# Optimization experiments

Measured on AMD Instinct MI355X. Metric: run time of the kernel, lower is better.

Reference implementation:

```python
import jax, jax.numpy as jnp
import numpy as np

DIM = 1024
NUM_HEADS = 16
HEAD_DIM = DIM // NUM_HEADS
B, L = 2, 2048


def setup_inputs() -> dict:
    key = jax.random.key(0)
    k_x, k_qkv, k_pw, k_pb = jax.random.split(key, 4)
    x = jax.random.normal(k_x, (B, L, DIM), dtype=jnp.float32)
    # nn.Linear(dim, 3*dim, bias=False): weight [3*dim, dim]; y = x @ W.T
    w_qkv = jax.random.normal(k_qkv, (3 * DIM, DIM), dtype=jnp.float32) * (DIM ** -0.5)
    # nn.Linear(dim, dim) with bias
    w_proj = jax.random.normal(k_pw, (DIM, DIM), dtype=jnp.float32) * (DIM ** -0.5)
    b_proj = jax.random.normal(k_pb, (DIM,), dtype=jnp.float32) * 0.01
    return {"x": x, "w_qkv": w_qkv, "w_proj": w_proj, "b_proj": b_proj}


def reference(x, w_qkv, w_proj, b_proj):
    Bx, Lx, C = x.shape
    qkv = x @ w_qkv.T  # [B, L, 3C]
    qkv = qkv.reshape(Bx, Lx, 3, NUM_HEADS, HEAD_DIM)
    q = jnp.transpose(qkv[:, :, 0], (0, 2, 1, 3))  # [B, H, L, D]
    k = jnp.transpose(qkv[:, :, 1], (0, 2, 1, 3))
    v = jnp.transpose(qkv[:, :, 2], (0, 2, 1, 3))
    attn = jnp.einsum('bhqd,bhkd->bhqk', q, k) * (HEAD_DIM ** -0.5)
    attn = jax.nn.softmax(attn, axis=-1)
    out = jnp.einsum('bhqk,bhkd->bhqd', attn, v)  # [B, H, L, D]
    out = jnp.transpose(out, (0, 2, 1, 3)).reshape(Bx, Lx, C)
    return out @ w_proj.T + b_proj
```

## Files before the change

### kernel.cpp

```cpp
#include <hip/hip_runtime.h>

#define DIM 1024
#define NH 16
#define HD 64
#define BB 2
#define LL 2048
#define BL (BB*LL)
#define NQKV (3*DIM)

typedef __bf16 bf16;
typedef __bf16 bf16x4 __attribute__((ext_vector_type(4)));
typedef __bf16 bf16x8 __attribute__((ext_vector_type(8)));
typedef float  f32x4  __attribute__((ext_vector_type(4)));

#define QSCALE 0.1803368801111204f

typedef __attribute__((address_space(3))) unsigned int lds_u32;
typedef __attribute__((address_space(1))) unsigned int glb_u32;

__device__ __forceinline__ void gld_lds16(const bf16* g, bf16* l) {
    __builtin_amdgcn_global_load_lds((const glb_u32*)g, (lds_u32*)l, 16, 0, 0);
}

#define C0 (BL*DIM/4)
#define C1 (NQKV*DIM/4)
#define C2 (DIM*DIM/4)
__global__ __launch_bounds__(256) void cvt_all(const float* __restrict__ x,
        const float* __restrict__ wq, const float* __restrict__ wp,
        bf16* __restrict__ xb, bf16* __restrict__ wqb, bf16* __restrict__ wpb) {
    int i = blockIdx.x * 256 + threadIdx.x;
    const float* in; bf16* out; int j;
    if (i < C0)            { in = x;  out = xb;  j = i; }
    else if (i < C0 + C1)  { in = wq; out = wqb; j = i - C0; }
    else                   { in = wp; out = wpb; j = i - C0 - C1; }
    float4 f = ((const float4*)in)[j];
    bf16x4 o = { (bf16)f.x, (bf16)f.y, (bf16)f.z, (bf16)f.w };
    ((bf16x4*)out)[j] = o;
}

__global__ __launch_bounds__(256, 3) void gemm_qkv(
        const bf16* __restrict__ A, const bf16* __restrict__ W,
        bf16* __restrict__ Qb, bf16* __restrict__ Kb, bf16* __restrict__ VTb) {
    __shared__ bf16 As[128][64];
    __shared__ bf16 Bs[128][64];
    const int tid = threadIdx.x;
    const int w = tid >> 6, lane = tid & 63, quad = lane >> 4, l16 = lane & 15;
    const int n0 = blockIdx.x * 128, m0 = blockIdx.y * 128;
    const int wm = (w & 1) * 64, wn = (w >> 1) * 64;
    f32x4 acc[4][4] = {};
    for (int k0 = 0; k0 < DIM; k0 += 64) {
        #pragma unroll
        for (int i = 0; i < 4; ++i) {
            int cb = w * 256 + i * 64;
            int gc = cb + lane;
            int r = gc >> 3;
            int cs = (gc & 7) ^ (r & 7);
            gld_lds16(A + (size_t)(m0 + r) * DIM + k0 + cs*8, &As[0][0] + cb * 8);
            gld_lds16(W + (size_t)(n0 + r) * DIM + k0 + cs*8, &Bs[0][0] + cb * 8);
        }
        __syncthreads();
        #pragma unroll
        for (int kc = 0; kc < 2; ++kc) {
            bf16x8 af[4], bfr[4];
            #pragma unroll
            for (int t = 0; t < 4; ++t) {
                int rw = wn + t*16 + l16;
                int cw = (kc*4 + quad) ^ (rw & 7);
                af[t] = *(const bf16x8*)(&Bs[0][0] + rw*64 + cw*8);
                int rx = wm + t*16 + l16;
                int cx = (kc*4 + quad) ^ (rx & 7);
                bfr[t] = *(const bf16x8*)(&As[0][0] + rx*64 + cx*8);
            }
            #pragma unroll
            for (int tm = 0; tm < 4; ++tm)
                #pragma unroll
                for (int tn = 0; tn < 4; ++tn)
                    acc[tm][tn] = __builtin_amdgcn_mfma_f32_16x16x32_bf16(
                                      af[tm], bfr[tn], acc[tm][tn], 0, 0, 0);
        }
        __syncthreads();
    }
    const int which = n0 >> 10;
    #pragma unroll
    for (int tm = 0; tm < 4; ++tm) {
        int nb = n0 + wn + tm*16 + quad*4;
        int rem = nb & 1023, h = rem >> 6, db = rem & 63;
        #pragma unroll
        for (int tn = 0; tn < 4; ++tn) {
            int m = m0 + wm + tn*16 + l16;
            int b = m >> 11, l = m & 2047, bh = (b << 4) | h;
            if (which == 0) {
                bf16x4 q4 = { (bf16)(acc[tm][tn][0] * QSCALE),
                              (bf16)(acc[tm][tn][1] * QSCALE),
                              (bf16)(acc[tm][tn][2] * QSCALE),
                              (bf16)(acc[tm][tn][3] * QSCALE) };
                *(bf16x4*)(Qb + ((size_t)bh << 17) + ((size_t)l << 6) + db) = q4;
            } else if (which == 1) {
                bf16x4 k4 = { (bf16)acc[tm][tn][0], (bf16)acc[tm][tn][1],
                              (bf16)acc[tm][tn][2], (bf16)acc[tm][tn][3] };
                *(bf16x4*)(Kb + ((size_t)bh << 17) + ((size_t)l << 6) + db) = k4;
            } else {
                #pragma unroll
                for (int r = 0; r < 4; ++r)
                    VTb[((size_t)bh << 17) + ((size_t)(db + r) << 11) + l] =
                        (bf16)acc[tm][tn][r];
            }
        }
    }
}

__global__ __launch_bounds__(256, 3) void gemm_proj(
        const bf16* __restrict__ A, const bf16* __restrict__ W,
        const float* __restrict__ bias, float* __restrict__ out) {
    __shared__ bf16 As[128][64];
    __shared__ bf16 Bs[64][64];
    const int tid = threadIdx.x;
    const int w = tid >> 6, lane = tid & 63, quad = lane >> 4, l16 = lane & 15;
    const int n0 = blockIdx.x * 64, m0 = blockIdx.y * 128;
    const int wm = (w & 1) * 64, wn = (w >> 1) * 32;
    f32x4 acc[2][4] = {};
    for (int k0 = 0; k0 < DIM; k0 += 64) {
        #pragma unroll
        for (int i = 0; i < 4; ++i) {
            int cb = w * 256 + i * 64;
            int gc = cb + lane;
            int r = gc >> 3;
            int cs = (gc & 7) ^ (r & 7);
            gld_lds16(A + (size_t)(m0 + r) * DIM + k0 + cs*8, &As[0][0] + cb * 8);
        }
        #pragma unroll
        for (int i = 0; i < 2; ++i) {
            int cb = w * 128 + i * 64;
            int gc = cb + lane;
            int r = gc >> 3;
            int cs = (gc & 7) ^ (r & 7);
            gld_lds16(W + (size_t)(n0 + r) * DIM + k0 + cs*8, &Bs[0][0] + cb * 8);
        }
        __syncthreads();
        #pragma unroll
        for (int kc = 0; kc < 2; ++kc) {
            bf16x8 af[2], bfr[4];
            #pragma unroll
            for (int t = 0; t < 2; ++t) {
                int rw = wn + t*16 + l16;
                int cw = (kc*4 + quad) ^ (rw & 7);
                af[t] = *(const bf16x8*)(&Bs[0][0] + rw*64 + cw*8);
            }
            #pragma unroll
            for (int t = 0; t < 4; ++t) {
                int rx = wm + t*16 + l16;
                int cx = (kc*4 + quad) ^ (rx & 7);
                bfr[t] = *(const bf16x8*)(&As[0][0] + rx*64 + cx*8);
            }
            #pragma unroll
            for (int tm = 0; tm < 2; ++tm)
                #pragma unroll
                for (int tn = 0; tn < 4; ++tn)
                    acc[tm][tn] = __builtin_amdgcn_mfma_f32_16x16x32_bf16(
                                      af[tm], bfr[tn], acc[tm][tn], 0, 0, 0);
        }
        __syncthreads();
    }
    #pragma unroll
    for (int tm = 0; tm < 2; ++tm) {
        int nb = n0 + wn + tm*16 + quad*4;
        float4 b4 = *(const float4*)&bias[nb];
        #pragma unroll
        for (int tn = 0; tn < 4; ++tn) {
            int m = m0 + wm + tn*16 + l16;
            float4 o4 = { acc[tm][tn][0] + b4.x, acc[tm][tn][1] + b4.y,
                          acc[tm][tn][2] + b4.z, acc[tm][tn][3] + b4.w };
            *(float4*)(out + (size_t)m * DIM + nb) = o4;
        }
    }
}

__global__ __launch_bounds__(256, 2) void attn(
        const bf16* __restrict__ Qb, const bf16* __restrict__ Kb,
        const bf16* __restrict__ VTb, bf16* __restrict__ AO) {
    __shared__ bf16 Ks[2][64][64];
    __shared__ bf16 VTs[2][64][64];
    __shared__ bf16 Ps[4][32][72];
    const int tid = threadIdx.x;
    const int w = tid >> 6, lane = tid & 63, quad = lane >> 4, l16 = lane & 15;
    const int qt = blockIdx.x, bh = blockIdx.y;
    const bf16* Qg = Qb + ((size_t)bh << 17) + (size_t)(qt * 128) * 64;
    const bf16* Kg = Kb + ((size_t)bh << 17);
    const bf16* Vg = VTb + ((size_t)bh << 17);

    bf16x8 aq[2][2];
    #pragma unroll
    for (int sub = 0; sub < 2; ++sub)
        #pragma unroll
        for (int kc = 0; kc < 2; ++kc)
            aq[sub][kc] = *(const bf16x8*)(Qg + (size_t)(w*32 + sub*16 + l16) * 64
                                           + kc*32 + quad*8);

    bf16x8 onesf = {};
    if (l16 == 0)
        #pragma unroll
        for (int j = 0; j < 8; ++j) onesf[j] = (bf16)1.0f;

    f32x4 oacc[2][4] = {};
    f32x4 lacc[2] = {};

    auto stage = [&](int kt, int buf) {
        #pragma unroll
        for (int i = 0; i < 2; ++i) {
            int gc = w*128 + i*64 + lane;
            int r = gc >> 3;
            int cs = (gc & 7) ^ (r & 7) ^ ((r >> 3) & 7);
            gld_lds16(Kg + (size_t)(kt*64 + r) * 64 + cs*8,
                      &Ks[buf][0][0] + (w*128 + i*64) * 8);
            gld_lds16(Vg + (size_t)r * 2048 + kt*64 + cs*8,
                      &VTs[buf][0][0] + (w*128 + i*64) * 8);
        }
    };

    stage(0, 0);
    for (int kt = 0; kt < 32; ++kt) {
        const int cur = kt & 1;
        __syncthreads();
        if (kt < 31) stage(kt + 1, cur ^ 1);

        f32x4 s[2][4] = {};
        #pragma unroll
        for (int kc = 0; kc < 2; ++kc)
            #pragma unroll
            for (int nt = 0; nt < 4; ++nt) {
                int row = 4*l16 + nt;
                int cp = (kc*4 + quad) ^ (row & 7) ^ ((row >> 3) & 7);
                bf16x8 bk = *(const bf16x8*)(&Ks[cur][0][0] + row*64 + cp*8);
                #pragma unroll
                for (int sub = 0; sub < 2; ++sub)
                    s[sub][nt] = __builtin_amdgcn_mfma_f32_16x16x32_bf16(
                                     aq[sub][kc], bk, s[sub][nt], 0, 0, 0);
            }

        #pragma unroll
        for (int sub = 0; sub < 2; ++sub)
            #pragma unroll
            for (int r = 0; r < 4; ++r) {
                bf16x4 p4 = { (bf16)exp2f(s[sub][0][r]), (bf16)exp2f(s[sub][1][r]),
                              (bf16)exp2f(s[sub][2][r]), (bf16)exp2f(s[sub][3][r]) };
                *(bf16x4*)&Ps[w][sub*16 + quad*4 + r][4*l16] = p4;
            }

        #pragma unroll
        for (int kc = 0; kc < 2; ++kc) {
            bf16x8 ap[2];
            #pragma unroll
            for (int sub = 0; sub < 2; ++sub)
                ap[sub] = *(const bf16x8*)&Ps[w][sub*16 + l16][kc*32 + quad*8];
            #pragma unroll
            for (int nt = 0; nt < 4; ++nt) {
                int row = nt*16 + l16;
                int cp = (kc*4 + quad) ^ (row & 7) ^ ((row >> 3) & 7);
                bf16x8 bv = *(const bf16x8*)(&VTs[cur][0][0] + row*64 + cp*8);
                #pragma unroll
                for (int sub = 0; sub < 2; ++sub)
                    oacc[sub][nt] = __builtin_amdgcn_mfma_f32_16x16x32_bf16(
                                        ap[sub], bv, oacc[sub][nt], 0, 0, 0);
            }
            #pragma unroll
            for (int sub = 0; sub < 2; ++sub)
                lacc[sub] = __builtin_amdgcn_mfma_f32_16x16x32_bf16(
                                ap[sub], onesf, lacc[sub], 0, 0, 0);
        }
    }

    const int b = bh >> 4, h = bh & 15;
    #pragma unroll
    for (int sub = 0; sub < 2; ++sub)
        #pragma unroll
        for (int r = 0; r < 4; ++r) {
            float l = __shfl(lacc[sub][r], quad * 16, 64);
            float inv = 1.0f / l;
            int lq = qt*128 + w*32 + sub*16 + quad*4 + r;
            size_t rowbase = ((size_t)(b * 2048 + lq)) * DIM + h * 64;
            #pragma unroll
            for (int nt = 0; nt < 4; ++nt)
                AO[rowbase + nt*16 + l16] = (bf16)(oacc[sub][nt][r] * inv);
        }
}

extern "C" void kernel_launch(void* const* d_in, const int* in_sizes, int n_in,
                              void* d_out, int out_size, void* d_ws, size_t ws_size,
                              hipStream_t stream) {
    const float* x      = (const float*)d_in[0];
    const float* w_qkv  = (const float*)d_in[1];
    const float* w_proj = (const float*)d_in[2];
    const float* b_proj = (const float*)d_in[3];
    float* out = (float*)d_out;
    char* ws = (char*)d_ws;

    bf16* xb  = (bf16*)(ws);
    bf16* wqb = (bf16*)(ws + ( 8u << 20));
    bf16* wpb = (bf16*)(ws + (14u << 20));
    bf16* Qb  = (bf16*)(ws + (16u << 20));
    bf16* Kb  = (bf16*)(ws + (24u << 20));
    bf16* VTb = (bf16*)(ws + (32u << 20));
    bf16* AOb = (bf16*)(ws + (40u << 20));

    cvt_all<<<(C0 + C1 + C2) / 256, 256, 0, stream>>>(x, w_qkv, w_proj, xb, wqb, wpb);
    gemm_qkv<<<dim3(NQKV/128, BL/128), 256, 0, stream>>>(xb, wqb, Qb, Kb, VTb);
    attn<<<dim3(LL/128, BB*NH),        256, 0, stream>>>(Qb, Kb, VTb, AOb);
    gemm_proj<<<dim3(DIM/64, BL/128),  256, 0, stream>>>(AOb, wpb, b_proj, out);
}
```

Measured before the change: 199.6 us.

## Split attention over key halves and combine partials in a normalization kernel

Attention blocks now each process half of the key sequence (grid z=2), writing unnormalized bf16 partial outputs and fp32 row sums; a new elementwise kernel adds the two halves and divides by the summed denominators before the projection GEMM. Launch bounds are raised to allow three blocks per CU. This aims to increase the number of concurrent attention blocks and improve GPU occupancy. It adds an extra kernel launch, extra global memory traffic for the partials, and rounding of unnormalized partials to bf16.

```diff
diff --git a/kernel.cpp b/kernel.cpp
--- a/kernel.cpp
+++ b/kernel.cpp
@@ -175,15 +175,20 @@
     }
 }
 
-__global__ __launch_bounds__(256, 2) void attn(
+__global__ __launch_bounds__(256, 3) void attn(
         const bf16* __restrict__ Qb, const bf16* __restrict__ Kb,
-        const bf16* __restrict__ VTb, bf16* __restrict__ AO) {
+        const bf16* __restrict__ VTb, bf16* __restrict__ OP0,
+        bf16* __restrict__ OP1, float* __restrict__ L0,
+        float* __restrict__ L1) {
     __shared__ bf16 Ks[2][64][64];
     __shared__ bf16 VTs[2][64][64];
     __shared__ bf16 Ps[4][32][72];
     const int tid = threadIdx.x;
     const int w = tid >> 6, lane = tid & 63, quad = lane >> 4, l16 = lane & 15;
-    const int qt = blockIdx.x, bh = blockIdx.y;
+    const int qt = blockIdx.x, bh = blockIdx.y, half = blockIdx.z;
+    const int k0t = half * 16;
+    bf16*  OPh = half ? OP1 : OP0;
+    float* Lh  = half ? L1 : L0;
     const bf16* Qg = Qb + ((size_t)bh << 17) + (size_t)(qt * 128) * 64;
     const bf16* Kg = Kb + ((size_t)bh << 17);
     const bf16* Vg = VTb + ((size_t)bh << 17);
@@ -217,11 +222,12 @@
         }
     };
 
-    stage(0, 0);
-    for (int kt = 0; kt < 32; ++kt) {
-        const int cur = kt & 1;
-        __syncthreads();
-        if (kt < 31) stage(kt + 1, cur ^ 1);
+    stage(k0t, 0);
+    for (int it = 0; it < 16; ++it) {
+        const int kt = k0t + it;
+        const int cur = it & 1;
+        __syncthreads();
+        if (it < 15) stage(kt + 1, cur ^ 1);
 
         f32x4 s[2][4] = {};
         #pragma unroll
@@ -274,14 +280,32 @@
     for (int sub = 0; sub < 2; ++sub)
         #pragma unroll
         for (int r = 0; r < 4; ++r) {
-            float l = __shfl(lacc[sub][r], quad * 16, 64);
-            float inv = 1.0f / l;
             int lq = qt*128 + w*32 + sub*16 + quad*4 + r;
+            if (l16 == 0)
+                Lh[((size_t)bh << 11) + lq] = lacc[sub][r];
             size_t rowbase = ((size_t)(b * 2048 + lq)) * DIM + h * 64;
             #pragma unroll
             for (int nt = 0; nt < 4; ++nt)
-                AO[rowbase + nt*16 + l16] = (bf16)(oacc[sub][nt][r] * inv);
-        }
+                OPh[rowbase + nt*16 + l16] = (bf16)oacc[sub][nt][r];
+        }
+}
+
+__global__ __launch_bounds__(256) void attn_norm(
+        bf16* __restrict__ OP0, const bf16* __restrict__ OP1,
+        const float* __restrict__ L0, const float* __restrict__ L1) {
+    int i = blockIdx.x * 256 + threadIdx.x;
+    int m = i >> 8, c4 = i & 255;
+    int b = m >> 11, lq = m & 2047, h = c4 >> 4;
+    size_t li = ((size_t)((b << 4) | h) << 11) + lq;
+    float inv = 1.0f / (L0[li] + L1[li]);
+    size_t off = ((size_t)m << 10) + c4 * 4;
+    bf16x4 a = *(const bf16x4*)(OP0 + off);
+    bf16x4 c = *(const bf16x4*)(OP1 + off);
+    bf16x4 o = { (bf16)(((float)a[0] + (float)c[0]) * inv),
+                 (bf16)(((float)a[1] + (float)c[1]) * inv),
+                 (bf16)(((float)a[2] + (float)c[2]) * inv),
+                 (bf16)(((float)a[3] + (float)c[3]) * inv) };
+    *(bf16x4*)(OP0 + off) = o;
 }
 
 extern "C" void kernel_launch(void* const* d_in, const int* in_sizes, int n_in,
@@ -300,10 +324,14 @@
     bf16* Qb  = (bf16*)(ws + (16u << 20));
     bf16* Kb  = (bf16*)(ws + (24u << 20));
     bf16* VTb = (bf16*)(ws + (32u << 20));
-    bf16* AOb = (bf16*)(ws + (40u << 20));
+    bf16* OP0 = (bf16*)(ws + (40u << 20));
+    bf16* OP1 = (bf16*)(ws + (48u << 20));
+    float* L0 = (float*)(ws + (56u << 20));
+    float* L1 = (float*)(ws + (57u << 20));
 
     cvt_all<<<(C0 + C1 + C2) / 256, 256, 0, stream>>>(x, w_qkv, w_proj, xb, wqb, wpb);
     gemm_qkv<<<dim3(NQKV/128, BL/128), 256, 0, stream>>>(xb, wqb, Qb, Kb, VTb);
-    attn<<<dim3(LL/128, BB*NH),        256, 0, stream>>>(Qb, Kb, VTb, AOb);
-    gemm_proj<<<dim3(DIM/64, BL/128),  256, 0, stream>>>(AOb, wpb, b_proj, out);
-}
+    attn<<<dim3(LL/128, BB*NH, 2), 256, 0, stream>>>(Qb, Kb, VTb, OP0, OP1, L0, L1);
+    attn_norm<<<BL*DIM/4/256, 256, 0, stream>>>(OP0, OP1, L0, L1);
+    gemm_proj<<<dim3(DIM/64, BL/128),  256, 0, stream>>>(OP0, wpb, b_proj, out);
+}
```

Measured after the change: 199.3 us. About the same (-0.2%).
